# Kernel optimization log

Measured on AMD Instinct MI355X. Metric: run time of the kernel, lower is better.

The kernel has to match this reference:

```python
import jax, jax.numpy as jnp
import numpy as np

N_NODES = 50000
N_EDGES = 800000
N_GRAPHS = 64
IN_CH = 128
HID = 128
PROC_X = 128
Q_DIM = 768
PROC_Q = 128
OUT_CH = 32


def setup_inputs() -> dict:
    key = jax.random.key(0)
    ks = jax.random.split(key, 16)
    inp = {
        "x": jax.random.normal(ks[0], (N_NODES, IN_CH), dtype=jnp.float32),
        "edge_index": jax.random.randint(ks[1], (2, N_EDGES), 0, N_NODES, dtype=jnp.int64),
        "batch": jnp.sort(jax.random.randint(ks[2], (N_NODES,), 0, N_GRAPHS, dtype=jnp.int64)),
        "question_embedding": jax.random.normal(ks[3], (N_GRAPHS, Q_DIM), dtype=jnp.float32),
    }
    s = 1.0 / np.sqrt(HID)
    inp["W0"] = jax.random.uniform(ks[4], (IN_CH, HID), minval=-s, maxval=s)
    inp["b0"] = jnp.zeros((HID,), jnp.float32)
    inp["W1"] = jax.random.uniform(ks[5], (HID, HID), minval=-s, maxval=s)
    inp["b1"] = jnp.zeros((HID,), jnp.float32)
    inp["W2"] = jax.random.uniform(ks[6], (HID, PROC_X), minval=-s, maxval=s)
    inp["b2"] = jnp.zeros((PROC_X,), jnp.float32)
    inp["fc0_w"] = jax.random.uniform(ks[7], (Q_DIM, PROC_Q), minval=-s, maxval=s)
    inp["fc0_b"] = jnp.zeros((PROC_Q,), jnp.float32)
    inp["fc1_w"] = jax.random.uniform(ks[8], (PROC_X + PROC_Q, HID), minval=-s, maxval=s)
    inp["fc1_b"] = jnp.zeros((HID,), jnp.float32)
    inp["fc2_w"] = jax.random.uniform(ks[9], (HID, OUT_CH), minval=-s, maxval=s)
    inp["fc2_b"] = jnp.zeros((OUT_CH,), jnp.float32)
    return inp


def _gcn_norm(edge_index, n_nodes):
    """Add self-loops and compute symmetric GCN normalization per edge."""
    loop = jnp.arange(n_nodes, dtype=edge_index.dtype)
    src = jnp.concatenate([edge_index[0], loop])
    dst = jnp.concatenate([edge_index[1], loop])
    ones = jnp.ones_like(dst, dtype=jnp.float32)
    deg = jax.ops.segment_sum(ones, dst, num_segments=n_nodes)
    dinv = jnp.where(deg > 0, jax.lax.rsqrt(deg), 0.0)
    norm = dinv[src] * dinv[dst]  # [E+N]
    return src, dst, norm


def _gcn_conv(x, src, dst, norm, W, b):
    h = x @ W                                # [N, F_out]
    msg = h[src] * norm[:, None]             # gather + scale  [E+N, F_out]
    agg = jax.ops.segment_sum(msg, dst, num_segments=x.shape[0])
    return agg + b


def reference(x, edge_index, batch, question_embedding,
              W0, b0, W1, b1, W2, b2,
              fc0_w, fc0_b, fc1_w, fc1_b, fc2_w, fc2_b):
    n = x.shape[0]
    src, dst, norm = _gcn_norm(edge_index, n)
    h = jax.nn.relu(_gcn_conv(x, src, dst, norm, W0, b0))
    h = jax.nn.relu(_gcn_conv(h, src, dst, norm, W1, b1))
    h = jax.nn.relu(_gcn_conv(h, src, dst, norm, W2, b2))
    q = jax.nn.relu(question_embedding @ fc0_w + fc0_b)  # [G, PROC_Q]
    q_exp = q[batch]                                      # [N, PROC_Q]
    combined = jnp.concatenate([h, q_exp], axis=1)
    out = jax.nn.relu(combined @ fc1_w + fc1_b)
    out = out @ fc2_w + fc2_b
    return out
```

## Files before the change

kernel.cpp:

```cpp
#include <hip/hip_runtime.h>
#include <hip/hip_bf16.h>

#define N_NODES 50000
#define N_EDGES 800000
#define N_GRAPHS 64
#define LSTR 136

typedef __attribute__((ext_vector_type(4))) short s4v;
typedef __attribute__((ext_vector_type(8))) short s8v;
typedef __attribute__((ext_vector_type(16))) float f16v;

struct HL { short hi, lo; };

__device__ inline HL bsplit(float f) {
    HL r;
    unsigned u = __float_as_uint(f);
    unsigned rh = (u + 0x7FFFu + ((u >> 16) & 1u)) >> 16;
    r.hi = (short)rh;
    float fh = __uint_as_float(rh << 16);
    float fl = f - fh;
    unsigned u2 = __float_as_uint(fl);
    unsigned rl = (u2 + 0x7FFFu + ((u2 >> 16) & 1u)) >> 16;
    r.lo = (short)rl;
    return r;
}

__device__ inline unsigned short f2bf(float f) {
    unsigned u = __float_as_uint(f);
    return (unsigned short)((u + 0x7FFFu + ((u >> 16) & 1u)) >> 16);
}

__device__ inline float bflo(unsigned u) { return __uint_as_float(u << 16); }
__device__ inline float bfhi(unsigned u) { return __uint_as_float(u & 0xFFFF0000u); }


__global__ __launch_bounds__(512) void k_scan_a(const int* __restrict__ cnt,
                                                int* __restrict__ rowptr,
                                                int* __restrict__ bsum,
                                                float* __restrict__ dinv, int n) {
    __shared__ int s[512];
    int t = threadIdx.x;
    int i = blockIdx.x * 512 + t;
    int v = (i < n) ? cnt[i] : 0;
    if (i < n) dinv[i] = rsqrtf((float)(v + 1));
    int pv = (v + 7) & ~7;
    s[t] = pv;
    __syncthreads();
    for (int d = 1; d < 512; d <<= 1) {
        int x = (t >= d) ? s[t - d] : 0;
        __syncthreads();
        s[t] += x;
        __syncthreads();
    }
    if (i < n) rowptr[i] = s[t] - pv;
    if (t == 511) bsum[blockIdx.x] = s[511];
}

__global__ __launch_bounds__(512) void k_scan_c(int* __restrict__ rowptr,
                                                const int* __restrict__ bsum,
                                                int n, int nb) {
    __shared__ int sb[128];
    int t = threadIdx.x;
    if (t < 128) sb[t] = (t < nb) ? bsum[t] : 0;
    __syncthreads();
    for (int d = 1; d < 128; d <<= 1) {
        int x = 0;
        if (t < 128 && t >= d) x = sb[t - d];
        __syncthreads();
        if (t < 128) sb[t] += x;
        __syncthreads();
    }
    int add = (blockIdx.x > 0) ? sb[blockIdx.x - 1] : 0;
    int i = blockIdx.x * 512 + t;
    if (i < n) rowptr[i] += add;
    if (i == 0) rowptr[n] = sb[nb - 1];
}

__global__ __launch_bounds__(512) void k_prep(const float* __restrict__ qe,
                                              const float* __restrict__ fc0w,
                                              const float* __restrict__ fc0b,
                                              const float* __restrict__ fc1w,
                                              const float* __restrict__ fc1b,
                                              const float* __restrict__ W0,
                                              const float* __restrict__ W1,
                                              const float* __restrict__ W2,
                                              const float* __restrict__ fc2w,
                                              const int* __restrict__ ei,
                                              int* __restrict__ cnt,
                                              int* __restrict__ rank,
                                              short* __restrict__ WH,
                                              short* __restrict__ WL,
                                              unsigned* __restrict__ Hsd,
                                              unsigned short* __restrict__ colA,
                                              float* __restrict__ qq, int E) {
    int b = blockIdx.x, tid = threadIdx.x;
    if (b >= 482) {
        int e = (b - 482) * 512 + tid;
        if (e < E) rank[e] = atomicAdd(&cnt[ei[E + e]], 1);
        return;
    }
    if (b == 481) {
        if (tid < 64) Hsd[(unsigned)N_NODES * 64u + tid] = 0u;
        if (tid >= 64 && tid < 128) Hsd[100001u * 64u + (unsigned)(tid - 64)] = 0u;
        return;
    }
    if (b >= 200) {
        int idx = (b - 200) * 512 + tid;
        if (idx < 143752) {
            uint4 p;
            p.x = p.y = p.z = p.w = 0xC350C350u;
            ((uint4*)colA)[idx] = p;
        }
        return;
    }
    if (b >= 64) {
        int i = (b - 64) * 512 + tid;
        float val;
        int dst;
        if (i < 65536) {
            int mat = i >> 14, off = i & 16383;
            int k = off >> 7, n = off & 127;
            const float* src = (mat == 0) ? W0 : (mat == 1) ? W1 : (mat == 2) ? W2 : fc1w;
            val = src[k * 128 + n];
            dst = mat * 16384 + n * 128 + k;
        } else {
            int off = i - 65536;
            int k = off >> 5, n = off & 31;
            val = fc2w[k * 32 + n];
            dst = 65536 + n * 128 + k;
        }
        HL r = bsplit(val);
        WH[dst] = r.hi;
        WL[dst] = r.lo;
        return;
    }
    __shared__ float qs[768];
    __shared__ float red[512];
    __shared__ float ql[128];
    const float* fc1bot = fc1w + 128 * 128;
    int g = b;
    for (int i = tid; i < 768; i += 512) qs[i] = qe[g * 768 + i];
    __syncthreads();
    int j = tid & 127, sl = tid >> 7;
    int kb = sl * 192;
    float a0 = 0, a1 = 0, a2 = 0, a3 = 0;
    for (int k = 0; k < 192; k += 4) {
        a0 += qs[kb + k + 0] * fc0w[(kb + k + 0) * 128 + j];
        a1 += qs[kb + k + 1] * fc0w[(kb + k + 1) * 128 + j];
        a2 += qs[kb + k + 2] * fc0w[(kb + k + 2) * 128 + j];
        a3 += qs[kb + k + 3] * fc0w[(kb + k + 3) * 128 + j];
    }
    red[tid] = (a0 + a1) + (a2 + a3);
    __syncthreads();
    if (tid < 128)
        ql[tid] = fmaxf(((red[tid] + red[tid + 128]) + (red[tid + 256] + red[tid + 384]))
                        + fc0b[tid], 0.f);
    __syncthreads();
    kb = sl * 32;
    float b0 = 0, b1 = 0;
    for (int k = 0; k < 32; k += 2) {
        b0 += ql[kb + k + 0] * fc1bot[(kb + k + 0) * 128 + j];
        b1 += ql[kb + k + 1] * fc1bot[(kb + k + 1) * 128 + j];
    }
    red[tid] = b0 + b1;
    __syncthreads();
    if (tid < 128)
        qq[g * 128 + tid] = ((red[tid] + red[tid + 128]) + (red[tid + 256] + red[tid + 384]))
                            + fc1b[tid];
}

__global__ __launch_bounds__(128) void k_fg(const float* __restrict__ A32,
                                            const short* __restrict__ WTh,
                                            const short* __restrict__ WTl,
                                            const float* __restrict__ dinv,
                                            unsigned short* __restrict__ oHs,
                                            const int* __restrict__ ei,
                                            const int* __restrict__ rowptr,
                                            const int* __restrict__ rank,
                                            unsigned short* __restrict__ colA,
                                            int nrows, int E, int GG) {
    const int tid = threadIdx.x;
    if (blockIdx.x >= GG) {
        int e = (blockIdx.x - GG) * 128 + tid;
        if (e < E) colA[rowptr[ei[E + e]] + rank[e]] = (unsigned short)ei[e];
        return;
    }
    __shared__ short Ah[32 * LSTR];
    const int row0 = blockIdx.x * 32;

    #pragma unroll
    for (int i = 0; i < 8; ++i) {
        int u = i * 128 + tid;
        int r = u >> 5, c4 = u & 31;
        int gr = row0 + r;
        float4 v = make_float4(0.f, 0.f, 0.f, 0.f);
        if (gr < nrows) v = ((const float4*)A32)[(size_t)gr * 32 + c4];
        s4v h4 = {(short)f2bf(v.x), (short)f2bf(v.y), (short)f2bf(v.z), (short)f2bf(v.w)};
        *(s4v*)&Ah[r * LSTR + c4 * 4] = h4;
    }
    __syncthreads();

    const int wv = tid >> 6, lane = tid & 63;
    const int m = lane & 31, half = lane >> 5;
    const int c0 = wv * 64 + m;
    f16v acc0 = {0.f}, acc1 = {0.f};
    #pragma unroll
    for (int ks = 0; ks < 8; ++ks) {
        int ko = ks * 16 + half * 8;
        s8v ah  = *(const s8v*)&Ah[m * LSTR + ko];
        s8v bh0 = *(const s8v*)&WTh[(size_t)c0 * 128 + ko];
        s8v bl0 = *(const s8v*)&WTl[(size_t)c0 * 128 + ko];
        s8v bh1 = *(const s8v*)&WTh[(size_t)(c0 + 32) * 128 + ko];
        s8v bl1 = *(const s8v*)&WTl[(size_t)(c0 + 32) * 128 + ko];
        acc0 = __builtin_amdgcn_mfma_f32_32x32x16_bf16(ah, bh0, acc0, 0, 0, 0);
        acc0 = __builtin_amdgcn_mfma_f32_32x32x16_bf16(ah, bl0, acc0, 0, 0, 0);
        acc1 = __builtin_amdgcn_mfma_f32_32x32x16_bf16(ah, bh1, acc1, 0, 0, 0);
        acc1 = __builtin_amdgcn_mfma_f32_32x32x16_bf16(ah, bl1, acc1, 0, 0, 0);
    }

    #pragma unroll
    for (int reg = 0; reg < 16; ++reg) {
        int rl = (reg & 3) + 8 * (reg >> 2) + 4 * half;
        int gr = row0 + rl;
        if (gr >= nrows) continue;
        float sc = dinv[gr];
        oHs[(size_t)gr * 128 + c0]      = f2bf(acc0[reg] * sc);
        oHs[(size_t)gr * 128 + c0 + 32] = f2bf(acc1[reg] * sc);
    }
}

template <int FC>
__global__ __launch_bounds__(256, 7) void k_gg(const unsigned* __restrict__ Hs,
                                               const int* __restrict__ rowptr,
                                               const unsigned short* __restrict__ colA,
                                               const float* __restrict__ dinv,
                                               const float* __restrict__ bias,
                                               const short* __restrict__ WTh,
                                               const short* __restrict__ WTl,
                                               const short* __restrict__ W2h,
                                               const short* __restrict__ W2l,
                                               const float* __restrict__ qq,
                                               const int* __restrict__ batch,
                                               const float* __restrict__ fc2b,
                                               unsigned short* __restrict__ oHs,
                                               float* __restrict__ out,
                                               int n) {
    __shared__ short SM[(FC ? 64 : 32) * LSTR];
    short* Ah = SM;
    const int tid = threadIdx.x;
    const int row0 = blockIdx.x * 32;
    const int wv = tid >> 6, l = tid & 63;
    const int m = l & 31, half = l >> 5;
    const int il = l & 15;
    const unsigned ilo = (unsigned)(il * 4);
    const unsigned shq = (l & 16) ? 16u : 0u;
    const bool qhi = (l & 32) != 0;
    const bool q0 = (l < 16);

    int pidx = row0 + wv * 8 + l;
    if (pidx > N_NODES) pidx = N_NODES;
    const int rp = rowptr[pidx];
    const int dvu = (int)__float_as_uint(dinv[pidx < N_NODES ? pidx : N_NODES - 1]);

    const float4 bA = ((const float4*)bias)[il * 2];
    const float4 bB = ((const float4*)bias)[il * 2 + 1];

    int node = row0 + wv * 8;
    int e0 = __builtin_amdgcn_readfirstlane(__builtin_amdgcn_readlane(rp, 0));
    int e1 = __builtin_amdgcn_readfirstlane(__builtin_amdgcn_readlane(rp, 1));
    bool alive = node < n;
    bool act = alive && (e0 < e1);
    uint4 cwA = {0, 0, 0, 0}, sf = {0, 0, 0, 0};
    if (alive) sf = *(const uint4*)(Hs + (unsigned)node * 64u + ilo);
    if (act)   cwA = *(const uint4*)(colA + e0);

    for (int i = 0; i < 8; ++i) {
        float a0 = 0, a1 = 0, a2 = 0, a3 = 0, a4 = 0, a5 = 0, a6 = 0, a7 = 0;
        float c0f = 0, c1f = 0, c2f = 0, c3f = 0, c4f = 0, c5f = 0, c6f = 0, c7f = 0;
        if (act) {
            const int ng = (e1 - e0) >> 3;
            uint4 cwB = *(const uint4*)(colA + e0 + ((ng > 1) ? 8 : 0));
            int g = 0;
            while (g + 2 <= ng) {
                uint4 nA = *(const uint4*)(colA + e0 + ((g + 2 < ng) ? (g + 2) * 8 : 0));
                uint4 nB = *(const uint4*)(colA + e0 + ((g + 3 < ng) ? (g + 3) * 8 : 0));
                unsigned wAa = qhi ? cwA.y : cwA.x;
                unsigned wAb = qhi ? cwA.w : cwA.z;
                unsigned wBa = qhi ? cwB.y : cwB.x;
                unsigned wBb = qhi ? cwB.w : cwB.z;
                uint4 va = *(const uint4*)(Hs + ((wAa >> shq) & 0xFFFFu) * 64u + ilo);
                uint4 vb = *(const uint4*)(Hs + ((wAb >> shq) & 0xFFFFu) * 64u + ilo);
                uint4 vc = *(const uint4*)(Hs + ((wBa >> shq) & 0xFFFFu) * 64u + ilo);
                uint4 vd = *(const uint4*)(Hs + ((wBb >> shq) & 0xFFFFu) * 64u + ilo);
                a0 += bflo(va.x); a1 += bfhi(va.x);
                a2 += bflo(va.y); a3 += bfhi(va.y);
                a4 += bflo(va.z); a5 += bfhi(va.z);
                a6 += bflo(va.w); a7 += bfhi(va.w);
                c0f += bflo(vb.x); c1f += bfhi(vb.x);
                c2f += bflo(vb.y); c3f += bfhi(vb.y);
                c4f += bflo(vb.z); c5f += bfhi(vb.z);
                c6f += bflo(vb.w); c7f += bfhi(vb.w);
                a0 += bflo(vc.x); a1 += bfhi(vc.x);
                a2 += bflo(vc.y); a3 += bfhi(vc.y);
                a4 += bflo(vc.z); a5 += bfhi(vc.z);
                a6 += bflo(vc.w); a7 += bfhi(vc.w);
                c0f += bflo(vd.x); c1f += bfhi(vd.x);
                c2f += bflo(vd.y); c3f += bfhi(vd.y);
                c4f += bflo(vd.z); c5f += bfhi(vd.z);
                c6f += bflo(vd.w); c7f += bfhi(vd.w);
                cwA = nA; cwB = nB; g += 2;
            }
            if (g < ng) {
                unsigned wAa = qhi ? cwA.y : cwA.x;
                unsigned wAb = qhi ? cwA.w : cwA.z;
                uint4 va = *(const uint4*)(Hs + ((wAa >> shq) & 0xFFFFu) * 64u + ilo);
                uint4 vb = *(const uint4*)(Hs + ((wAb >> shq) & 0xFFFFu) * 64u + ilo);
                a0 += bflo(va.x); a1 += bfhi(va.x);
                a2 += bflo(va.y); a3 += bfhi(va.y);
                a4 += bflo(va.z); a5 += bfhi(va.z);
                a6 += bflo(va.w); a7 += bfhi(va.w);
                c0f += bflo(vb.x); c1f += bfhi(vb.x);
                c2f += bflo(vb.y); c3f += bfhi(vb.y);
                c4f += bflo(vb.z); c5f += bfhi(vb.z);
                c6f += bflo(vb.w); c7f += bfhi(vb.w);
            }
        }
        float s0 = a0 + c0f, s1 = a1 + c1f, s2 = a2 + c2f, s3 = a3 + c3f;
        float s4 = a4 + c4f, s5 = a5 + c5f, s6 = a6 + c6f, s7 = a7 + c7f;

        int e0n = e1;
        int e1n = (i < 7) ? __builtin_amdgcn_readfirstlane(__builtin_amdgcn_readlane(rp, i + 2)) : 0;
        int noden = node + 1;
        bool aliven = (i < 7) && (noden < n);
        bool actn = aliven && (e0n < e1n);
        uint4 cwn = {0, 0, 0, 0}, sfn = {0, 0, 0, 0};
        if (aliven) sfn = *(const uint4*)(Hs + (unsigned)noden * 64u + ilo);
        if (actn)   cwn = *(const uint4*)(colA + e0n);

        const int r = wv * 8 + i;
        if (alive) {
            s0 += __shfl_xor(s0, 16); s1 += __shfl_xor(s1, 16);
            s2 += __shfl_xor(s2, 16); s3 += __shfl_xor(s3, 16);
            s4 += __shfl_xor(s4, 16); s5 += __shfl_xor(s5, 16);
            s6 += __shfl_xor(s6, 16); s7 += __shfl_xor(s7, 16);
            s0 += __shfl_xor(s0, 32); s1 += __shfl_xor(s1, 32);
            s2 += __shfl_xor(s2, 32); s3 += __shfl_xor(s3, 32);
            s4 += __shfl_xor(s4, 32); s5 += __shfl_xor(s5, 32);
            s6 += __shfl_xor(s6, 32); s7 += __shfl_xor(s7, 32);
            float di = __uint_as_float((unsigned)__builtin_amdgcn_readlane(dvu, i));
            float o0 = fmaxf((s0 + bflo(sf.x)) * di + bA.x, 0.f);
            float o1 = fmaxf((s1 + bfhi(sf.x)) * di + bA.y, 0.f);
            float o2 = fmaxf((s2 + bflo(sf.y)) * di + bA.z, 0.f);
            float o3 = fmaxf((s3 + bfhi(sf.y)) * di + bA.w, 0.f);
            float o4 = fmaxf((s4 + bflo(sf.z)) * di + bB.x, 0.f);
            float o5 = fmaxf((s5 + bfhi(sf.z)) * di + bB.y, 0.f);
            float o6 = fmaxf((s6 + bflo(sf.w)) * di + bB.z, 0.f);
            float o7 = fmaxf((s7 + bfhi(sf.w)) * di + bB.w, 0.f);
            if (q0) {
                uint4 pk;
                pk.x = (unsigned)f2bf(o0) | ((unsigned)f2bf(o1) << 16);
                pk.y = (unsigned)f2bf(o2) | ((unsigned)f2bf(o3) << 16);
                pk.z = (unsigned)f2bf(o4) | ((unsigned)f2bf(o5) << 16);
                pk.w = (unsigned)f2bf(o6) | ((unsigned)f2bf(o7) << 16);
                *(uint4*)&Ah[r * LSTR + il * 8] = pk;
            }
        } else if (q0) {
            uint4 z = {0, 0, 0, 0};
            *(uint4*)&Ah[r * LSTR + il * 8] = z;
        }
        e0 = e0n; e1 = e1n; cwA = cwn; sf = sfn;
        act = actn; alive = aliven; node = noden;
    }
    __syncthreads();

    const int c0 = wv * 32 + m;
    f16v acc = {0.f};
    #pragma unroll
    for (int ks = 0; ks < 8; ++ks) {
        int ko = ks * 16 + half * 8;
        s8v ah = *(const s8v*)&Ah[m * LSTR + ko];
        s8v bh = *(const s8v*)&WTh[(size_t)c0 * 128 + ko];
        s8v bl = *(const s8v*)&WTl[(size_t)c0 * 128 + ko];
        acc = __builtin_amdgcn_mfma_f32_32x32x16_bf16(ah, bh, acc, 0, 0, 0);
        acc = __builtin_amdgcn_mfma_f32_32x32x16_bf16(ah, bl, acc, 0, 0, 0);
    }

    if (FC == 0) {
        #pragma unroll
        for (int reg = 0; reg < 16; ++reg) {
            int rl = (reg & 3) + 8 * (reg >> 2) + 4 * half;
            int gr = row0 + rl;
            if (gr >= n) continue;
            oHs[(size_t)gr * 128 + c0] = f2bf(acc[reg] * dinv[gr]);
        }
    } else {
        short* Pl = SM + 32 * LSTR;
        __syncthreads();
        #pragma unroll
        for (int reg = 0; reg < 16; ++reg) {
            int rl = (reg & 3) + 8 * (reg >> 2) + 4 * half;
            int gr = row0 + rl;
            int g = (gr < n) ? batch[gr] : 0;
            float v = fmaxf(acc[reg] + qq[(size_t)g * 128 + c0], 0.f);
            HL p = bsplit(v);
            Ah[rl * LSTR + c0] = p.hi;
            Pl[rl * LSTR + c0] = p.lo;
        }
        __syncthreads();
        f16v acc2 = {0.f};
        #pragma unroll
        for (int ks = 0; ks < 2; ++ks) {
            int ko = wv * 32 + ks * 16 + half * 8;
            s8v ah = *(const s8v*)&Ah[m * LSTR + ko];
            s8v al = *(const s8v*)&Pl[m * LSTR + ko];
            s8v bh = *(const s8v*)&W2h[(size_t)m * 128 + ko];
            s8v bl = *(const s8v*)&W2l[(size_t)m * 128 + ko];
            acc2 = __builtin_amdgcn_mfma_f32_32x32x16_bf16(ah, bh, acc2, 0, 0, 0);
            acc2 = __builtin_amdgcn_mfma_f32_32x32x16_bf16(ah, bl, acc2, 0, 0, 0);
            acc2 = __builtin_amdgcn_mfma_f32_32x32x16_bf16(al, bh, acc2, 0, 0, 0);
        }
        __syncthreads();
        float* red = (float*)SM;
        if (wv > 0) {
            #pragma unroll
            for (int reg = 0; reg < 16; ++reg) {
                int rl = (reg & 3) + 8 * (reg >> 2) + 4 * half;
                red[(wv - 1) * 1056 + rl * 33 + m] = acc2[reg];
            }
        }
        __syncthreads();
        if (wv == 0) {
            #pragma unroll
            for (int reg = 0; reg < 16; ++reg) {
                int rl = (reg & 3) + 8 * (reg >> 2) + 4 * half;
                int gr = row0 + rl;
                if (gr < n)
                    out[(size_t)gr * 32 + m] = acc2[reg]
                        + (red[rl * 33 + m] + red[1056 + rl * 33 + m])
                        + red[2112 + rl * 33 + m] + fc2b[m];
            }
        }
    }
}


extern "C" void kernel_launch(void* const* d_in, const int* in_sizes, int n_in,
                              void* d_out, int out_size, void* d_ws, size_t ws_size,
                              hipStream_t stream) {
    const float* x    = (const float*)d_in[0];
    const int*   ei   = (const int*)d_in[1];
    const int*   batch= (const int*)d_in[2];
    const float* qe   = (const float*)d_in[3];
    const float* W0   = (const float*)d_in[4];
    const float* b0   = (const float*)d_in[5];
    const float* W1   = (const float*)d_in[6];
    const float* b1   = (const float*)d_in[7];
    const float* W2   = (const float*)d_in[8];
    const float* b2   = (const float*)d_in[9];
    const float* fc0w = (const float*)d_in[10];
    const float* fc0b = (const float*)d_in[11];
    const float* fc1w = (const float*)d_in[12];
    const float* fc1b = (const float*)d_in[13];
    const float* fc2w = (const float*)d_in[14];
    const float* fc2b = (const float*)d_in[15];
    float* out = (float*)d_out;

    float* WS = (float*)d_ws;
    unsigned short* HS  = (unsigned short*)WS;
    unsigned short* HS2 = (unsigned short*)(WS + 3200064);
    float* DINV = WS + 6400128;
    float* QQ   = WS + 6450144;
    int*   CNT  = (int*)(WS + 6458336);
    int*   ROWPTR = (int*)(WS + 6508352);
    int*   RANK = (int*)(WS + 6558368);
    unsigned short* COL = (unsigned short*)(WS + 7358368);
    int*   BSUM = (int*)(WS + 7933376);
    short* WTH  = (short*)(WS + 7933504);
    short* WTL  = WTH + 69632;

    const int N = N_NODES, E = N_EDGES;
    const int sb = (N + 511) / 512;
    const int gg = (N + 31) / 32;
    const int histb = (E + 511) / 512;
    const int fillb = (E + 127) / 128;

    (void)hipMemsetAsync(CNT, 0, N * sizeof(int), stream);
    k_prep<<<482 + histb, 512, 0, stream>>>(qe, fc0w, fc0b, fc1w, fc1b,
                                            W0, W1, W2, fc2w, ei, CNT, RANK,
                                            WTH, WTL, (unsigned*)HS, COL, QQ, E);
    k_scan_a<<<sb, 512, 0, stream>>>(CNT, ROWPTR, BSUM, DINV, N);
    k_scan_c<<<sb, 512, 0, stream>>>(ROWPTR, BSUM, N, sb);
    k_fg<<<gg + fillb, 128, 0, stream>>>(x, WTH, WTL, DINV, HS,
                                         ei, ROWPTR, RANK, COL, N, E, gg);
    k_gg<0><<<gg, 256, 0, stream>>>((const unsigned*)HS, ROWPTR, COL, DINV, b0,
                                    WTH + 16384, WTL + 16384, nullptr, nullptr,
                                    nullptr, nullptr, nullptr, HS2, nullptr, N);
    k_gg<0><<<gg, 256, 0, stream>>>((const unsigned*)HS2, ROWPTR, COL, DINV, b1,
                                    WTH + 32768, WTL + 32768, nullptr, nullptr,
                                    nullptr, nullptr, nullptr, HS, nullptr, N);
    k_gg<1><<<gg, 256, 0, stream>>>((const unsigned*)HS, ROWPTR, COL, DINV, b2,
                                    WTH + 49152, WTL + 49152, WTH + 65536, WTL + 65536,
                                    QQ, batch, fc2b, nullptr, out, N);
}
```

Measured before the change: 306.1 us.

## Privatize degree histogram into 8 partitioned counters to cut atomic contention

The per-destination degree histogram now goes into 8 separate counter arrays, picked by block index, which spreads the atomic traffic. The rank stores the partition id in its high bits. The scan kernel computes per-partition base offsets so the CSR fill can still place each edge at a unique slot. The counters reuse the HS2 buffer as scratch, and the change adds a larger memset plus extra base8 reads and writes. Launch bounds for k_gg also go from 7 to 8 waves per EU, which tightens the register budget.

```diff
diff --git a/kernel.cpp b/kernel.cpp
--- a/kernel.cpp
+++ b/kernel.cpp
@@ -5,6 +5,7 @@
 #define N_EDGES 800000
 #define N_GRAPHS 64
 #define LSTR 136
+#define NP 50016
 
 typedef __attribute__((ext_vector_type(4))) short s4v;
 typedef __attribute__((ext_vector_type(8))) short s8v;
@@ -34,16 +35,27 @@
 __device__ inline float bfhi(unsigned u) { return __uint_as_float(u & 0xFFFF0000u); }
 
 
-__global__ __launch_bounds__(512) void k_scan_a(const int* __restrict__ cnt,
+__global__ __launch_bounds__(512) void k_scan_a(const int* __restrict__ cnt8,
                                                 int* __restrict__ rowptr,
                                                 int* __restrict__ bsum,
-                                                float* __restrict__ dinv, int n) {
+                                                float* __restrict__ dinv,
+                                                int* __restrict__ base8, int n) {
     __shared__ int s[512];
     int t = threadIdx.x;
     int i = blockIdx.x * 512 + t;
-    int v = (i < n) ? cnt[i] : 0;
-    if (i < n) dinv[i] = rsqrtf((float)(v + 1));
-    int pv = (v + 7) & ~7;
+    int deg = 0;
+    if (i < n) {
+        int b = 0;
+        #pragma unroll
+        for (int p = 0; p < 8; ++p) {
+            int c = cnt8[p * NP + i];
+            base8[p * NP + i] = b;
+            b += c;
+        }
+        deg = b;
+        dinv[i] = rsqrtf((float)(deg + 1));
+    }
+    int pv = (deg + 7) & ~7;
     s[t] = pv;
     __syncthreads();
     for (int d = 1; d < 512; d <<= 1) {
@@ -86,7 +98,7 @@
                                               const float* __restrict__ W2,
                                               const float* __restrict__ fc2w,
                                               const int* __restrict__ ei,
-                                              int* __restrict__ cnt,
+                                              int* __restrict__ cnt8,
                                               int* __restrict__ rank,
                                               short* __restrict__ WH,
                                               short* __restrict__ WL,
@@ -96,7 +108,12 @@
     int b = blockIdx.x, tid = threadIdx.x;
     if (b >= 482) {
         int e = (b - 482) * 512 + tid;
-        if (e < E) rank[e] = atomicAdd(&cnt[ei[E + e]], 1);
+        if (e < E) {
+            int dst = ei[E + e];
+            int p = b & 7;
+            int r = atomicAdd(&cnt8[p * NP + dst], 1);
+            rank[e] = (p << 24) | r;
+        }
         return;
     }
     if (b == 481) {
@@ -177,12 +194,18 @@
                                             const int* __restrict__ ei,
                                             const int* __restrict__ rowptr,
                                             const int* __restrict__ rank,
+                                            const int* __restrict__ base8,
                                             unsigned short* __restrict__ colA,
                                             int nrows, int E, int GG) {
     const int tid = threadIdx.x;
     if (blockIdx.x >= GG) {
         int e = (blockIdx.x - GG) * 128 + tid;
-        if (e < E) colA[rowptr[ei[E + e]] + rank[e]] = (unsigned short)ei[e];
+        if (e < E) {
+            int dst = ei[E + e];
+            int rk = rank[e];
+            int p = rk >> 24, r = rk & 0xFFFFFF;
+            colA[rowptr[dst] + base8[p * NP + dst] + r] = (unsigned short)ei[e];
+        }
         return;
     }
     __shared__ short Ah[32 * LSTR];
@@ -230,7 +253,7 @@
 }
 
 template <int FC>
-__global__ __launch_bounds__(256, 7) void k_gg(const unsigned* __restrict__ Hs,
+__global__ __launch_bounds__(256, 8) void k_gg(const unsigned* __restrict__ Hs,
                                                const int* __restrict__ rowptr,
                                                const unsigned short* __restrict__ colA,
                                                const float* __restrict__ dinv,
@@ -470,13 +493,14 @@
     unsigned short* HS2 = (unsigned short*)(WS + 3200064);
     float* DINV = WS + 6400128;
     float* QQ   = WS + 6450144;
-    int*   CNT  = (int*)(WS + 6458336);
     int*   ROWPTR = (int*)(WS + 6508352);
     int*   RANK = (int*)(WS + 6558368);
     unsigned short* COL = (unsigned short*)(WS + 7358368);
     int*   BSUM = (int*)(WS + 7933376);
     short* WTH  = (short*)(WS + 7933504);
     short* WTL  = WTH + 69632;
+    int*   CNT8  = (int*)HS2;
+    int*   BASE8 = CNT8 + 8 * NP;
 
     const int N = N_NODES, E = N_EDGES;
     const int sb = (N + 511) / 512;
@@ -484,14 +508,14 @@
     const int histb = (E + 511) / 512;
     const int fillb = (E + 127) / 128;
 
-    (void)hipMemsetAsync(CNT, 0, N * sizeof(int), stream);
+    (void)hipMemsetAsync(CNT8, 0, 8 * NP * sizeof(int), stream);
     k_prep<<<482 + histb, 512, 0, stream>>>(qe, fc0w, fc0b, fc1w, fc1b,
-                                            W0, W1, W2, fc2w, ei, CNT, RANK,
+                                            W0, W1, W2, fc2w, ei, CNT8, RANK,
                                             WTH, WTL, (unsigned*)HS, COL, QQ, E);
-    k_scan_a<<<sb, 512, 0, stream>>>(CNT, ROWPTR, BSUM, DINV, N);
+    k_scan_a<<<sb, 512, 0, stream>>>(CNT8, ROWPTR, BSUM, DINV, BASE8, N);
     k_scan_c<<<sb, 512, 0, stream>>>(ROWPTR, BSUM, N, sb);
     k_fg<<<gg + fillb, 128, 0, stream>>>(x, WTH, WTL, DINV, HS,
-                                         ei, ROWPTR, RANK, COL, N, E, gg);
+                                         ei, ROWPTR, RANK, BASE8, COL, N, E, gg);
     k_gg<0><<<gg, 256, 0, stream>>>((const unsigned*)HS, ROWPTR, COL, DINV, b0,
                                     WTH + 16384, WTL + 16384, nullptr, nullptr,
                                     nullptr, nullptr, nullptr, HS2, nullptr, N);
```

Result: slower. 347.0 us (+13.4%).
